# Kernel optimization log

Hardware: AMD Instinct MI355X
Metric: run time of the kernel (lower is better)

## Reference

```python
import jax, jax.numpy as jnp
import numpy as np

B, T, F1, F2 = 16384, 5, 300, 251
IN, H = 551, 128

def setup_inputs() -> dict:
    key = jax.random.key(0)
    ks = jax.random.split(key, 16)
    s = 0.05
    return {
        "x1": jax.random.normal(ks[0], (B, T, F1), jnp.float32),
        "x2": jax.random.normal(ks[1], (B, T, F2), jnp.float32),
        "W_ih": jax.random.normal(ks[2], (4 * H, IN), jnp.float32) * s,
        "W_hh": jax.random.normal(ks[3], (4 * H, H), jnp.float32) * s,
        "b_ih": jax.random.normal(ks[4], (4 * H,), jnp.float32) * s,
        "b_hh": jax.random.normal(ks[5], (4 * H,), jnp.float32) * s,
        "W1": jax.random.normal(ks[6], (531, H * T), jnp.float32) * s,
        "b1": jax.random.normal(ks[7], (531,), jnp.float32) * s,
        "W2": jax.random.normal(ks[8], (256, 531), jnp.float32) * s,
        "b2": jax.random.normal(ks[9], (256,), jnp.float32) * s,
        "W3": jax.random.normal(ks[10], (64, 256), jnp.float32) * s,
        "b3": jax.random.normal(ks[11], (64,), jnp.float32) * s,
        "W4": jax.random.normal(ks[12], (2, 64), jnp.float32) * s,
        "b4": jax.random.normal(ks[13], (2,), jnp.float32) * s,
    }

def _lstm(x, W_ih, W_hh, b_ih, b_hh):
    # x: [B, T, IN] -> outputs [B, T, H]; PyTorch gate order i, f, g, o
    xg = jnp.einsum('bti,gi->btg', x, W_ih) + b_ih + b_hh  # [B, T, 4H]
    xg = jnp.transpose(xg, (1, 0, 2))  # [T, B, 4H]
    h0 = jnp.zeros((x.shape[0], H), x.dtype)
    c0 = jnp.zeros((x.shape[0], H), x.dtype)

    def step(carry, xg_t):
        h, c = carry
        g = xg_t + h @ W_hh.T  # [B, 4H]
        i, f, gg, o = jnp.split(g, 4, axis=-1)
        c = jax.nn.sigmoid(f) * c + jax.nn.sigmoid(i) * jnp.tanh(gg)
        h = jax.nn.sigmoid(o) * jnp.tanh(c)
        return (h, c), h

    _, hs = jax.lax.scan(step, (h0, c0), xg)  # hs: [T, B, H]
    return jnp.transpose(hs, (1, 0, 2))

def reference(x1, x2, W_ih, W_hh, b_ih, b_hh, W1, b1, W2, b2, W3, b3, W4, b4):
    x = jnp.concatenate((x1, x2), axis=2)  # [B, T, 551]
    h = _lstm(x, W_ih, W_hh, b_ih, b_hh)   # [B, T, H]
    h = h.reshape(h.shape[0], T * H)
    h = jax.nn.relu(h @ W1.T + b1)
    h = jax.nn.relu(h @ W2.T + b2)
    h = jax.nn.relu(h @ W3.T + b3)
    logits = h @ W4.T + b4
    return jax.nn.softmax(logits, axis=1)
```

## Files before the change

### kernel.cpp

```cpp
#include <hip/hip_runtime.h>
#include <hip/hip_bf16.h>


typedef short  short8  __attribute__((ext_vector_type(8)));
typedef short  short4v __attribute__((ext_vector_type(4)));
typedef float  f32x4   __attribute__((ext_vector_type(4)));

#define MFMA(a, b, c) __builtin_amdgcn_mfma_f32_16x16x32_bf16((a), (b), (c), 0, 0, 0)

__device__ __forceinline__ short f2bs(float f) {
    __hip_bfloat16 h = __float2bfloat16(f);
    union { __hip_bfloat16 h; short s; } u; u.h = h; return u.s;
}
__device__ __forceinline__ float b2f(short s) {
    union { unsigned u; float f; } v; v.u = ((unsigned)(unsigned short)s) << 16; return v.f;
}
__device__ __forceinline__ float sigf(float x)  { return 1.f / (1.f + __expf(-x)); }
__device__ __forceinline__ float mytanh(float x){ return 2.f / (1.f + __expf(-2.f * x)) - 1.f; }

#define BB     16384
#define TT     5
#define F1     300
#define F2     251
#define INF    551
#define KP     576
#define G4     512
#define HH     128
#define FLAT   640
#define L1N    531
#define L1P    576
#define L1KP   544
#define L2N    256
#define L3N    64

#define O_WIH  0u
#define O_WHH  589824u
#define O_W1   720896u
#define O_W2   1458176u
#define O_W3   1736704u
#define O_BG   1769472u
#define O_B1   1771520u
#define O_XG   1773824u
#define O_HS   85659904u
#define WS_NEED 106631424u

__device__ __forceinline__ void pack_b(const float* __restrict__ W, short* __restrict__ dst,
                                       int i, int tpn, int Nsrc, int Ksrc, int ldw)
{
    int tile = i >> 9, rem = i & 511, lane = rem >> 3, jj = rem & 7;
    int tn = tile / tpn, tk = tile - tn * tpn;
    int n = tn * 16 + (lane & 15);
    int k = tk * 32 + (lane >> 4) * 8 + jj;
    float v = (n < Nsrc && k < Ksrc) ? W[n * ldw + k] : 0.f;
    dst[i] = f2bs(v);
}

__global__ void prep_kernel(
    const float* __restrict__ W_ih, const float* __restrict__ W_hh,
    const float* __restrict__ b_ih, const float* __restrict__ b_hh,
    const float* __restrict__ W1,   const float* __restrict__ b1,
    const float* __restrict__ W2,   const float* __restrict__ W3,
    short* __restrict__ Wihp, short* __restrict__ Whhp, float* __restrict__ biasg,
    short* __restrict__ W1p,  float* __restrict__ b1p,  short* __restrict__ W2p,
    short* __restrict__ W3p)
{
    const int N0 = G4 * KP;
    const int N1 = N0 + G4 * HH;
    const int N2 = N1 + L1P * FLAT;
    const int N3 = N2 + L2N * L1KP;
    const int N4 = N3 + L3N * L2N;
    const int N5 = N4 + G4;
    const int N6 = N5 + L1P;
    const int stride = gridDim.x * blockDim.x;
    for (int i = blockIdx.x * blockDim.x + threadIdx.x; i < N6; i += stride) {
        if (i < N0)      pack_b(W_ih, Wihp, i,       18, G4,  INF, INF);
        else if (i < N1) pack_b(W_hh, Whhp, i - N0,   4, G4,  HH,  HH);
        else if (i < N2) pack_b(W1,   W1p,  i - N1,  20, L1N, FLAT, FLAT);
        else if (i < N3) pack_b(W2,   W2p,  i - N2,  17, L2N, L1N, L1N);
        else if (i < N4) pack_b(W3,   W3p,  i - N3,   8, L3N, L2N, L2N);
        else if (i < N5) { int j = i - N4; biasg[j] = b_ih[j] + b_hh[j]; }
        else             { int j = i - N5; b1p[j] = (j < L1N) ? b1[j] : 0.f; }
    }
}

__device__ __forceinline__ float4 load_chunk4(const float* __restrict__ x1,
                                              const float* __restrict__ x2,
                                              int brow, int t, int c)
{
    if (c < F1) {
        return *(const float4*)(x1 + (brow * TT + t) * F1 + c);
    }
    float4 r;
    int base = (brow * TT + t) * F2 + (c - F1);
    r.x = (c + 0 < INF) ? x2[base + 0] : 0.f;
    r.y = (c + 1 < INF) ? x2[base + 1] : 0.f;
    r.z = (c + 2 < INF) ? x2[base + 2] : 0.f;
    r.w = (c + 3 < INF) ? x2[base + 3] : 0.f;
    return r;
}

__global__ __launch_bounds__(512, 4) void k1_xgemm(
    const float* __restrict__ x1, const float* __restrict__ x2,
    const short* __restrict__ Wihp, const float* __restrict__ biasg,
    short* __restrict__ xg)
{
    __shared__ __align__(16) short At[64][296];
    const int tid  = threadIdx.x;
    const int w    = tid >> 6;
    const int lane = tid & 63;
    const int quad = lane >> 4;
    const int c16  = lane & 15;
    const int m0   = blockIdx.x * 64;
    const int t    = m0 >> 14;
    const int bb   = m0 & 16383;

    f32x4 acc[4][4];
#pragma unroll
    for (int mt = 0; mt < 4; ++mt)
#pragma unroll
        for (int nt = 0; nt < 4; ++nt)
            acc[mt][nt] = (f32x4){0.f, 0.f, 0.f, 0.f};

    const int srow  = tid >> 3;
    const int kslot = tid & 7;

    for (int half = 0; half < 2; ++half) {
        __syncthreads();
        {
            int brow = bb + srow;
#pragma unroll
            for (int c = 0; c < 9; ++c) {
                int kl = c * 32 + kslot * 4;
                float4 v = load_chunk4(x1, x2, brow, t, half * 288 + kl);
                short4v s;
                s[0] = f2bs(v.x); s[1] = f2bs(v.y); s[2] = f2bs(v.z); s[3] = f2bs(v.w);
                *(short4v*)&At[srow][kl] = s;
            }
        }
        __syncthreads();
#pragma unroll
        for (int ks = 0; ks < 9; ++ks) {
            short8 a[4];
#pragma unroll
            for (int mt = 0; mt < 4; ++mt)
                a[mt] = *(const short8*)&At[mt * 16 + c16][ks * 32 + quad * 8];
#pragma unroll
            for (int nt = 0; nt < 4; ++nt) {
                int tk = half * 9 + ks;
                short8 b = *(const short8*)&Wihp[(((w * 4 + nt) * 18 + tk) << 9) + lane * 8];
#pragma unroll
                for (int mt = 0; mt < 4; ++mt)
                    acc[mt][nt] = MFMA(a[mt], b, acc[mt][nt]);
            }
        }
    }
#pragma unroll
    for (int nt = 0; nt < 4; ++nt) {
        float bv = biasg[w * 64 + nt * 16 + c16];
#pragma unroll
        for (int mt = 0; mt < 4; ++mt) {
            short4v o;
#pragma unroll
            for (int r = 0; r < 4; ++r) o[r] = f2bs(acc[mt][nt][r] + bv);
            int tm = (m0 >> 4) + mt, tn = w * 4 + nt;
            *(short4v*)&xg[((tm * 32 + tn) << 8) + lane * 4] = o;
        }
    }
}

__global__ __launch_bounds__(512, 2) void k2_rec(
    const short* __restrict__ Whhp, const short* __restrict__ xg,
    short* __restrict__ hs)
{
    __shared__ __align__(16) short hb[2][32][136];
    const int tid  = threadIdx.x;
    const int w    = tid >> 6;
    const int lane = tid & 63;
    const int quad = lane >> 4;
    const int c16  = lane & 15;
    const int btile = blockIdx.x * 2;

    short8 bfr[4][4];
#pragma unroll
    for (int g = 0; g < 4; ++g)
#pragma unroll
        for (int ks = 0; ks < 4; ++ks)
            bfr[g][ks] = *(const short8*)&Whhp[((((g * 8 + w) * 4) + ks) << 9) + lane * 8];

    float cst[2][4];
#pragma unroll
    for (int mt = 0; mt < 2; ++mt)
#pragma unroll
        for (int r = 0; r < 4; ++r) cst[mt][r] = 0.f;

    const int j = w * 16 + c16;

    for (int t = 0; t < TT; ++t) {
        short4v xq[2][4];
#pragma unroll
        for (int mt = 0; mt < 2; ++mt)
#pragma unroll
            for (int g = 0; g < 4; ++g)
                xq[mt][g] = *(const short4v*)
                    &xg[((((t << 10) + btile + mt) * 32 + (g * 8 + w)) << 8) + lane * 4];

        f32x4 acc[2][4];
#pragma unroll
        for (int mt = 0; mt < 2; ++mt)
#pragma unroll
            for (int g = 0; g < 4; ++g)
                acc[mt][g] = (f32x4){0.f, 0.f, 0.f, 0.f};

        if (t > 0) {
            const short (*cur)[136] = hb[(t - 1) & 1];
#pragma unroll
            for (int ks = 0; ks < 4; ++ks) {
                short8 a[2];
#pragma unroll
                for (int mt = 0; mt < 2; ++mt)
                    a[mt] = *(const short8*)&cur[mt * 16 + c16][ks * 32 + quad * 8];
#pragma unroll
                for (int mt = 0; mt < 2; ++mt)
#pragma unroll
                    for (int g = 0; g < 4; ++g)
                        acc[mt][g] = MFMA(a[mt], bfr[g][ks], acc[mt][g]);
            }
        }

        short (*nxt)[136] = hb[t & 1];
#pragma unroll
        for (int mt = 0; mt < 2; ++mt) {
#pragma unroll
            for (int r = 0; r < 4; ++r) {
                int m = mt * 16 + quad * 4 + r;
                float gi = acc[mt][0][r] + b2f(xq[mt][0][r]);
                float gf = acc[mt][1][r] + b2f(xq[mt][1][r]);
                float gg = acc[mt][2][r] + b2f(xq[mt][2][r]);
                float go = acc[mt][3][r] + b2f(xq[mt][3][r]);
                float cn = sigf(gf) * cst[mt][r] + sigf(gi) * mytanh(gg);
                cst[mt][r] = cn;
                nxt[m][j] = f2bs(sigf(go) * mytanh(cn));
            }
        }
        __syncthreads();
        {
            int tm = w >> 2, kt = w & 3;
            short8 v = *(const short8*)&nxt[tm * 16 + c16][kt * 32 + quad * 8];
            *(short8*)&hs[(((btile + tm) * 20 + t * 4 + kt) << 9) + lane * 8] = v;
        }
    }
}

__global__ __launch_bounds__(256, 2) void mlp_kernel(
    const short* __restrict__ hs,
    const short* __restrict__ W1p, const float* __restrict__ b1p,
    const short* __restrict__ W2p, const float* __restrict__ b2,
    const short* __restrict__ W3p, const float* __restrict__ b3,
    const float* __restrict__ W4,  const float* __restrict__ b4,
    float* __restrict__ out)
{
    __shared__ __align__(16) short a1[32][584];
    __shared__ __align__(16) short a2[32][264];
    __shared__ __align__(16) short a3[32][72];
    const int tid  = threadIdx.x;
    const int w    = tid >> 6;
    const int lane = tid & 63;
    const int quad = lane >> 4;
    const int c16  = lane & 15;
    const int m0   = blockIdx.x * 32;
    const int mtile = blockIdx.x * 2;

    {
        f32x4 acc[2][9];
#pragma unroll
        for (int mt = 0; mt < 2; ++mt)
#pragma unroll
            for (int i = 0; i < 9; ++i)
                acc[mt][i] = (f32x4){0.f, 0.f, 0.f, 0.f};
#pragma unroll 4
        for (int ks = 0; ks < 20; ++ks) {
            short8 a[2];
#pragma unroll
            for (int mt = 0; mt < 2; ++mt)
                a[mt] = *(const short8*)&hs[(((mtile + mt) * 20 + ks) << 9) + lane * 8];
#pragma unroll
            for (int i = 0; i < 9; ++i) {
                short8 b = *(const short8*)&W1p[(((w * 9 + i) * 20 + ks) << 9) + lane * 8];
                acc[0][i] = MFMA(a[0], b, acc[0][i]);
                acc[1][i] = MFMA(a[1], b, acc[1][i]);
            }
        }
#pragma unroll
        for (int i = 0; i < 9; ++i) {
            int n = (w * 9 + i) * 16 + c16;
            float bv = b1p[n];
#pragma unroll
            for (int mt = 0; mt < 2; ++mt)
#pragma unroll
                for (int r = 0; r < 4; ++r) {
                    int m = mt * 16 + quad * 4 + r;
                    float v = acc[mt][i][r] + bv;
                    a1[m][n] = f2bs(v > 0.f ? v : 0.f);
                }
        }
    }
    __syncthreads();

    {
        f32x4 acc[2][4];
#pragma unroll
        for (int mt = 0; mt < 2; ++mt)
#pragma unroll
            for (int i = 0; i < 4; ++i)
                acc[mt][i] = (f32x4){0.f, 0.f, 0.f, 0.f};
#pragma unroll 4
        for (int ks = 0; ks < 17; ++ks) {
            short8 a[2];
#pragma unroll
            for (int mt = 0; mt < 2; ++mt)
                a[mt] = *(const short8*)&a1[mt * 16 + c16][ks * 32 + quad * 8];
#pragma unroll
            for (int i = 0; i < 4; ++i) {
                short8 b = *(const short8*)&W2p[(((w * 4 + i) * 17 + ks) << 9) + lane * 8];
                acc[0][i] = MFMA(a[0], b, acc[0][i]);
                acc[1][i] = MFMA(a[1], b, acc[1][i]);
            }
        }
#pragma unroll
        for (int i = 0; i < 4; ++i) {
            int n = (w * 4 + i) * 16 + c16;
            float bv = b2[n];
#pragma unroll
            for (int mt = 0; mt < 2; ++mt)
#pragma unroll
                for (int r = 0; r < 4; ++r) {
                    int m = mt * 16 + quad * 4 + r;
                    float v = acc[mt][i][r] + bv;
                    a2[m][n] = f2bs(v > 0.f ? v : 0.f);
                }
        }
    }
    __syncthreads();

    {
        f32x4 acc[2];
        acc[0] = (f32x4){0.f, 0.f, 0.f, 0.f};
        acc[1] = (f32x4){0.f, 0.f, 0.f, 0.f};
#pragma unroll
        for (int ks = 0; ks < 8; ++ks) {
            short8 a[2];
#pragma unroll
            for (int mt = 0; mt < 2; ++mt)
                a[mt] = *(const short8*)&a2[mt * 16 + c16][ks * 32 + quad * 8];
            short8 b = *(const short8*)&W3p[((w * 8 + ks) << 9) + lane * 8];
            acc[0] = MFMA(a[0], b, acc[0]);
            acc[1] = MFMA(a[1], b, acc[1]);
        }
        int n = w * 16 + c16;
        float bv = b3[n];
#pragma unroll
        for (int mt = 0; mt < 2; ++mt)
#pragma unroll
            for (int r = 0; r < 4; ++r) {
                int m = mt * 16 + quad * 4 + r;
                float v = acc[mt][r] + bv;
                a3[m][n] = f2bs(v > 0.f ? v : 0.f);
            }
    }
    __syncthreads();

    if (tid < 64) {
        int m   = tid >> 1;
        int cls = tid & 1;
        float s = b4[cls];
#pragma unroll 8
        for (int k = 0; k < 64; ++k)
            s += b2f(a3[m][k]) * W4[cls * 64 + k];
        float other = __shfl_xor(s, 1);
        float p = 1.f / (1.f + __expf(other - s));
        out[(m0 + m) * 2 + cls] = p;
    }
}

extern "C" void kernel_launch(void* const* d_in, const int* in_sizes, int n_in,
                              void* d_out, int out_size, void* d_ws, size_t ws_size,
                              hipStream_t stream)
{
    (void)in_sizes; (void)n_in; (void)out_size;
    if (ws_size < (size_t)WS_NEED) return;

    const float* x1   = (const float*)d_in[0];
    const float* x2   = (const float*)d_in[1];
    const float* W_ih = (const float*)d_in[2];
    const float* W_hh = (const float*)d_in[3];
    const float* b_ih = (const float*)d_in[4];
    const float* b_hh = (const float*)d_in[5];
    const float* W1   = (const float*)d_in[6];
    const float* b1   = (const float*)d_in[7];
    const float* W2   = (const float*)d_in[8];
    const float* b2   = (const float*)d_in[9];
    const float* W3   = (const float*)d_in[10];
    const float* b3   = (const float*)d_in[11];
    const float* W4   = (const float*)d_in[12];
    const float* b4   = (const float*)d_in[13];

    char* ws = (char*)d_ws;
    short* Wihp  = (short*)(ws + O_WIH);
    short* Whhp  = (short*)(ws + O_WHH);
    short* W1p   = (short*)(ws + O_W1);
    short* W2p   = (short*)(ws + O_W2);
    short* W3p   = (short*)(ws + O_W3);
    float* biasg = (float*)(ws + O_BG);
    float* b1p   = (float*)(ws + O_B1);
    short* xg    = (short*)(ws + O_XG);
    short* hsb   = (short*)(ws + O_HS);

    prep_kernel<<<3461, 256, 0, stream>>>(W_ih, W_hh, b_ih, b_hh, W1, b1, W2, W3,
                                          Wihp, Whhp, biasg, W1p, b1p, W2p, W3p);
    k1_xgemm<<<1280, 512, 0, stream>>>(x1, x2, Wihp, biasg, xg);
    k2_rec<<<512, 512, 0, stream>>>(Whhp, xg, hsb);
    mlp_kernel<<<512, 256, 0, stream>>>(hsb, W1p, b1p, W2p, b2, W3p, b3, W4, b4,
                                        (float*)d_out);
}
```

Before: 366.6 us.

## Fuse LSTM recurrence and MLP head into one kernel with shared-memory hidden states

Merges the recurrent LSTM kernel and the MLP kernel into a single 512-thread kernel. The hidden-state sequence stays in LDS instead of making a round trip through a global workspace buffer, and one kernel launch is removed. The MLP stage is re-split so that 8 waves cover two 16-row M tiles by four N groups. Shared memory is aliased across phases, which needs extra barriers, and the larger LDS footprint (about 78KB) may reduce occupancy.

```diff
diff --git a/kernel.cpp b/kernel.cpp
--- a/kernel.cpp
+++ b/kernel.cpp
@@ -41,8 +41,7 @@
 #define O_BG   1769472u
 #define O_B1   1771520u
 #define O_XG   1773824u
-#define O_HS   85659904u
-#define WS_NEED 106631424u
+#define WS_NEED 85659904u
 
 __device__ __forceinline__ void pack_b(const float* __restrict__ W, short* __restrict__ dst,
                                        int i, int tpn, int Nsrc, int Ksrc, int ldw)
@@ -168,204 +167,177 @@
     }
 }
 
-__global__ __launch_bounds__(512, 2) void k2_rec(
+__global__ __launch_bounds__(512, 2) void k2mlp_kernel(
     const short* __restrict__ Whhp, const short* __restrict__ xg,
-    short* __restrict__ hs)
-{
-    __shared__ __align__(16) short hb[2][32][136];
+    const short* __restrict__ W1p, const float* __restrict__ b1p,
+    const short* __restrict__ W2p, const float* __restrict__ b2,
+    const short* __restrict__ W3p, const float* __restrict__ b3,
+    const float* __restrict__ W4,  const float* __restrict__ b4,
+    float* __restrict__ out)
+{
+    __shared__ __align__(16) char smem[78336];
+    short* hsL = (short*)smem;
+    short (*a2)[264] = (short (*)[264])smem;
+    short (*hb0)[136] = (short (*)[136])(smem + 40960);
+    short (*hb1)[136] = (short (*)[136])(smem + 40960 + 8704);
+    short (*a1)[584] = (short (*)[584])(smem + 40960);
+    short (*a3)[72]  = (short (*)[72])(smem + 40960);
+
     const int tid  = threadIdx.x;
     const int w    = tid >> 6;
     const int lane = tid & 63;
     const int quad = lane >> 4;
     const int c16  = lane & 15;
     const int btile = blockIdx.x * 2;
-
-    short8 bfr[4][4];
-#pragma unroll
-    for (int g = 0; g < 4; ++g)
-#pragma unroll
-        for (int ks = 0; ks < 4; ++ks)
-            bfr[g][ks] = *(const short8*)&Whhp[((((g * 8 + w) * 4) + ks) << 9) + lane * 8];
-
-    float cst[2][4];
-#pragma unroll
-    for (int mt = 0; mt < 2; ++mt)
-#pragma unroll
-        for (int r = 0; r < 4; ++r) cst[mt][r] = 0.f;
-
-    const int j = w * 16 + c16;
-
-    for (int t = 0; t < TT; ++t) {
-        short4v xq[2][4];
+    const int m0    = blockIdx.x * 32;
+
+    {
+        short8 bfr[4][4];
+#pragma unroll
+        for (int g = 0; g < 4; ++g)
+#pragma unroll
+            for (int ks = 0; ks < 4; ++ks)
+                bfr[g][ks] = *(const short8*)&Whhp[((((g * 8 + w) * 4) + ks) << 9) + lane * 8];
+
+        float cst[2][4];
 #pragma unroll
         for (int mt = 0; mt < 2; ++mt)
 #pragma unroll
-            for (int g = 0; g < 4; ++g)
-                xq[mt][g] = *(const short4v*)
-                    &xg[((((t << 10) + btile + mt) * 32 + (g * 8 + w)) << 8) + lane * 4];
-
-        f32x4 acc[2][4];
-#pragma unroll
-        for (int mt = 0; mt < 2; ++mt)
-#pragma unroll
-            for (int g = 0; g < 4; ++g)
-                acc[mt][g] = (f32x4){0.f, 0.f, 0.f, 0.f};
-
-        if (t > 0) {
-            const short (*cur)[136] = hb[(t - 1) & 1];
-#pragma unroll
-            for (int ks = 0; ks < 4; ++ks) {
-                short8 a[2];
-#pragma unroll
-                for (int mt = 0; mt < 2; ++mt)
-                    a[mt] = *(const short8*)&cur[mt * 16 + c16][ks * 32 + quad * 8];
-#pragma unroll
-                for (int mt = 0; mt < 2; ++mt)
-#pragma unroll
-                    for (int g = 0; g < 4; ++g)
-                        acc[mt][g] = MFMA(a[mt], bfr[g][ks], acc[mt][g]);
-            }
-        }
-
-        short (*nxt)[136] = hb[t & 1];
-#pragma unroll
-        for (int mt = 0; mt < 2; ++mt) {
-#pragma unroll
-            for (int r = 0; r < 4; ++r) {
-                int m = mt * 16 + quad * 4 + r;
-                float gi = acc[mt][0][r] + b2f(xq[mt][0][r]);
-                float gf = acc[mt][1][r] + b2f(xq[mt][1][r]);
-                float gg = acc[mt][2][r] + b2f(xq[mt][2][r]);
-                float go = acc[mt][3][r] + b2f(xq[mt][3][r]);
-                float cn = sigf(gf) * cst[mt][r] + sigf(gi) * mytanh(gg);
-                cst[mt][r] = cn;
-                nxt[m][j] = f2bs(sigf(go) * mytanh(cn));
-            }
-        }
-        __syncthreads();
-        {
-            int tm = w >> 2, kt = w & 3;
-            short8 v = *(const short8*)&nxt[tm * 16 + c16][kt * 32 + quad * 8];
-            *(short8*)&hs[(((btile + tm) * 20 + t * 4 + kt) << 9) + lane * 8] = v;
-        }
-    }
-}
-
-__global__ __launch_bounds__(256, 2) void mlp_kernel(
-    const short* __restrict__ hs,
-    const short* __restrict__ W1p, const float* __restrict__ b1p,
-    const short* __restrict__ W2p, const float* __restrict__ b2,
-    const short* __restrict__ W3p, const float* __restrict__ b3,
-    const float* __restrict__ W4,  const float* __restrict__ b4,
-    float* __restrict__ out)
-{
-    __shared__ __align__(16) short a1[32][584];
-    __shared__ __align__(16) short a2[32][264];
-    __shared__ __align__(16) short a3[32][72];
-    const int tid  = threadIdx.x;
-    const int w    = tid >> 6;
-    const int lane = tid & 63;
-    const int quad = lane >> 4;
-    const int c16  = lane & 15;
-    const int m0   = blockIdx.x * 32;
-    const int mtile = blockIdx.x * 2;
+            for (int r = 0; r < 4; ++r) cst[mt][r] = 0.f;
+
+        const int j = w * 16 + c16;
+
+        for (int t = 0; t < TT; ++t) {
+            short4v xq[2][4];
+#pragma unroll
+            for (int mt = 0; mt < 2; ++mt)
+#pragma unroll
+                for (int g = 0; g < 4; ++g)
+                    xq[mt][g] = *(const short4v*)
+                        &xg[((((t << 10) + btile + mt) * 32 + (g * 8 + w)) << 8) + lane * 4];
+
+            f32x4 acc[2][4];
+#pragma unroll
+            for (int mt = 0; mt < 2; ++mt)
+#pragma unroll
+                for (int g = 0; g < 4; ++g)
+                    acc[mt][g] = (f32x4){0.f, 0.f, 0.f, 0.f};
+
+            if (t > 0) {
+                const short (*cur)[136] = ((t - 1) & 1) ? hb1 : hb0;
+#pragma unroll
+                for (int ks = 0; ks < 4; ++ks) {
+                    short8 a[2];
+#pragma unroll
+                    for (int mt = 0; mt < 2; ++mt)
+                        a[mt] = *(const short8*)&cur[mt * 16 + c16][ks * 32 + quad * 8];
+#pragma unroll
+                    for (int mt = 0; mt < 2; ++mt)
+#pragma unroll
+                        for (int g = 0; g < 4; ++g)
+                            acc[mt][g] = MFMA(a[mt], bfr[g][ks], acc[mt][g]);
+                }
+            }
+
+            short (*nxt)[136] = (t & 1) ? hb1 : hb0;
+#pragma unroll
+            for (int mt = 0; mt < 2; ++mt) {
+#pragma unroll
+                for (int r = 0; r < 4; ++r) {
+                    int m = mt * 16 + quad * 4 + r;
+                    float gi = acc[mt][0][r] + b2f(xq[mt][0][r]);
+                    float gf = acc[mt][1][r] + b2f(xq[mt][1][r]);
+                    float gg = acc[mt][2][r] + b2f(xq[mt][2][r]);
+                    float go = acc[mt][3][r] + b2f(xq[mt][3][r]);
+                    float cn = sigf(gf) * cst[mt][r] + sigf(gi) * mytanh(gg);
+                    cst[mt][r] = cn;
+                    nxt[m][j] = f2bs(sigf(go) * mytanh(cn));
+                }
+            }
+            __syncthreads();
+            {
+                int tm = w >> 2, kt = w & 3;
+                short8 v = *(const short8*)&nxt[tm * 16 + c16][kt * 32 + quad * 8];
+                *(short8*)&hsL[((tm * 20 + t * 4 + kt) << 9) + lane * 8] = v;
+            }
+        }
+    }
+    __syncthreads();
+
+    const int mh = w >> 2, wn = w & 3;
 
     {
-        f32x4 acc[2][9];
-#pragma unroll
-        for (int mt = 0; mt < 2; ++mt)
-#pragma unroll
-            for (int i = 0; i < 9; ++i)
-                acc[mt][i] = (f32x4){0.f, 0.f, 0.f, 0.f};
+        f32x4 acc1[9];
+#pragma unroll
+        for (int i = 0; i < 9; ++i) acc1[i] = (f32x4){0.f, 0.f, 0.f, 0.f};
 #pragma unroll 4
         for (int ks = 0; ks < 20; ++ks) {
-            short8 a[2];
-#pragma unroll
-            for (int mt = 0; mt < 2; ++mt)
-                a[mt] = *(const short8*)&hs[(((mtile + mt) * 20 + ks) << 9) + lane * 8];
+            short8 a = *(const short8*)&hsL[((mh * 20 + ks) << 9) + lane * 8];
 #pragma unroll
             for (int i = 0; i < 9; ++i) {
-                short8 b = *(const short8*)&W1p[(((w * 9 + i) * 20 + ks) << 9) + lane * 8];
-                acc[0][i] = MFMA(a[0], b, acc[0][i]);
-                acc[1][i] = MFMA(a[1], b, acc[1][i]);
-            }
-        }
+                short8 b = *(const short8*)&W1p[(((wn * 9 + i) * 20 + ks) << 9) + lane * 8];
+                acc1[i] = MFMA(a, b, acc1[i]);
+            }
+        }
+        __syncthreads();
 #pragma unroll
         for (int i = 0; i < 9; ++i) {
-            int n = (w * 9 + i) * 16 + c16;
+            int n = (wn * 9 + i) * 16 + c16;
             float bv = b1p[n];
 #pragma unroll
-            for (int mt = 0; mt < 2; ++mt)
-#pragma unroll
-                for (int r = 0; r < 4; ++r) {
-                    int m = mt * 16 + quad * 4 + r;
-                    float v = acc[mt][i][r] + bv;
-                    a1[m][n] = f2bs(v > 0.f ? v : 0.f);
-                }
+            for (int r = 0; r < 4; ++r) {
+                int m = mh * 16 + quad * 4 + r;
+                float v = acc1[i][r] + bv;
+                a1[m][n] = f2bs(v > 0.f ? v : 0.f);
+            }
         }
     }
     __syncthreads();
 
     {
-        f32x4 acc[2][4];
-#pragma unroll
-        for (int mt = 0; mt < 2; ++mt)
-#pragma unroll
-            for (int i = 0; i < 4; ++i)
-                acc[mt][i] = (f32x4){0.f, 0.f, 0.f, 0.f};
+        f32x4 acc2[4];
+#pragma unroll
+        for (int i = 0; i < 4; ++i) acc2[i] = (f32x4){0.f, 0.f, 0.f, 0.f};
 #pragma unroll 4
         for (int ks = 0; ks < 17; ++ks) {
-            short8 a[2];
-#pragma unroll
-            for (int mt = 0; mt < 2; ++mt)
-                a[mt] = *(const short8*)&a1[mt * 16 + c16][ks * 32 + quad * 8];
+            short8 a = *(const short8*)&a1[mh * 16 + c16][ks * 32 + quad * 8];
 #pragma unroll
             for (int i = 0; i < 4; ++i) {
-                short8 b = *(const short8*)&W2p[(((w * 4 + i) * 17 + ks) << 9) + lane * 8];
-                acc[0][i] = MFMA(a[0], b, acc[0][i]);
-                acc[1][i] = MFMA(a[1], b, acc[1][i]);
+                short8 b = *(const short8*)&W2p[(((wn * 4 + i) * 17 + ks) << 9) + lane * 8];
+                acc2[i] = MFMA(a, b, acc2[i]);
             }
         }
 #pragma unroll
         for (int i = 0; i < 4; ++i) {
-            int n = (w * 4 + i) * 16 + c16;
+            int n = (wn * 4 + i) * 16 + c16;
             float bv = b2[n];
 #pragma unroll
-            for (int mt = 0; mt < 2; ++mt)
-#pragma unroll
-                for (int r = 0; r < 4; ++r) {
-                    int m = mt * 16 + quad * 4 + r;
-                    float v = acc[mt][i][r] + bv;
-                    a2[m][n] = f2bs(v > 0.f ? v : 0.f);
-                }
+            for (int r = 0; r < 4; ++r) {
+                int m = mh * 16 + quad * 4 + r;
+                float v = acc2[i][r] + bv;
+                a2[m][n] = f2bs(v > 0.f ? v : 0.f);
+            }
         }
     }
     __syncthreads();
 
     {
-        f32x4 acc[2];
-        acc[0] = (f32x4){0.f, 0.f, 0.f, 0.f};
-        acc[1] = (f32x4){0.f, 0.f, 0.f, 0.f};
+        f32x4 acc3 = (f32x4){0.f, 0.f, 0.f, 0.f};
 #pragma unroll
         for (int ks = 0; ks < 8; ++ks) {
-            short8 a[2];
-#pragma unroll
-            for (int mt = 0; mt < 2; ++mt)
-                a[mt] = *(const short8*)&a2[mt * 16 + c16][ks * 32 + quad * 8];
-            short8 b = *(const short8*)&W3p[((w * 8 + ks) << 9) + lane * 8];
-            acc[0] = MFMA(a[0], b, acc[0]);
-            acc[1] = MFMA(a[1], b, acc[1]);
-        }
-        int n = w * 16 + c16;
+            short8 a = *(const short8*)&a2[mh * 16 + c16][ks * 32 + quad * 8];
+            short8 b = *(const short8*)&W3p[((wn * 8 + ks) << 9) + lane * 8];
+            acc3 = MFMA(a, b, acc3);
+        }
+        __syncthreads();
+        int n = wn * 16 + c16;
         float bv = b3[n];
 #pragma unroll
-        for (int mt = 0; mt < 2; ++mt)
-#pragma unroll
-            for (int r = 0; r < 4; ++r) {
-                int m = mt * 16 + quad * 4 + r;
-                float v = acc[mt][r] + bv;
-                a3[m][n] = f2bs(v > 0.f ? v : 0.f);
-            }
+        for (int r = 0; r < 4; ++r) {
+            int m = mh * 16 + quad * 4 + r;
+            float v = acc3[r] + bv;
+            a3[m][n] = f2bs(v > 0.f ? v : 0.f);
+        }
     }
     __syncthreads();
 
@@ -413,12 +385,10 @@
     float* biasg = (float*)(ws + O_BG);
     float* b1p   = (float*)(ws + O_B1);
     short* xg    = (short*)(ws + O_XG);
-    short* hsb   = (short*)(ws + O_HS);
 
     prep_kernel<<<3461, 256, 0, stream>>>(W_ih, W_hh, b_ih, b_hh, W1, b1, W2, W3,
                                           Wihp, Whhp, biasg, W1p, b1p, W2p, W3p);
     k1_xgemm<<<1280, 512, 0, stream>>>(x1, x2, Wihp, biasg, xg);
-    k2_rec<<<512, 512, 0, stream>>>(Whhp, xg, hsb);
-    mlp_kernel<<<512, 256, 0, stream>>>(hsb, W1p, b1p, W2p, b2, W3p, b3, W4, b4,
-                                        (float*)d_out);
-}
+    k2mlp_kernel<<<512, 512, 0, stream>>>(Whhp, xg, W1p, b1p, W2p, b2, W3p, b3,
+                                          W4, b4, (float*)d_out);
+}
```

Result: slower. 399.0 us (+8.8%).
